# Performance work log

Hardware: AMD Instinct MI355X
Metric: run time of the kernel (lower is better)

## Reference

```python
import jax, jax.numpy as jnp
import numpy as np

IN_C, OUT_C, K, STRIDE, PAD, N_EXPERTS = 64, 128, 3, 1, 1, 4
B, H, W = 32, 64, 64


def setup_inputs() -> dict:
    key = jax.random.key(0)
    k1, k2, k3, k4 = jax.random.split(key, 4)
    x = jax.random.normal(k1, (B, IN_C, H, W), dtype=jnp.float32)
    idx = jax.random.randint(k2, (B,), 0, N_EXPERTS, dtype=jnp.int64)
    # Expert conv weights/biases (PyTorch Conv2d layout: [out_c, in_c, kh, kw])
    fan_in = IN_C * K * K
    bound = 1.0 / np.sqrt(fan_in)
    Wc = jax.random.uniform(k3, (N_EXPERTS, OUT_C, IN_C, K, K), dtype=jnp.float32,
                            minval=-bound, maxval=bound)
    bc = jax.random.uniform(k4, (N_EXPERTS, OUT_C), dtype=jnp.float32,
                            minval=-bound, maxval=bound)
    return {"x": x, "idx": idx, "Wc": Wc, "bc": bc}


def _conv2d(x, w, b):
    # x: [B, C_in, H, W], w: [C_out, C_in, K, K], b: [C_out]
    y = jax.lax.conv_general_dilated(
        x, w,
        window_strides=(STRIDE, STRIDE),
        padding=[(PAD, PAD), (PAD, PAD)],
        dimension_numbers=("NCHW", "OIHW", "NCHW"),
    )
    return y + b[None, :, None, None]


def reference(x, idx, Wc, bc):
    # Compute every expert's conv for every sample (faithful to the torch code),
    # then gather each sample's selected expert output.
    results = jax.vmap(lambda w, b: _conv2d(x, w, b))(Wc, bc)  # [E, B, C_out, H, W]
    results = jnp.moveaxis(results, 0, 1)                      # [B, E, C_out, H, W]
    out = jnp.take_along_axis(
        results, idx[:, None, None, None, None].astype(jnp.int32), axis=1
    )  # [B, 1, C_out, H, W]
    return jnp.squeeze(out, axis=1)
```

## Files before the change

kernel.cpp:

```cpp
#include <hip/hip_runtime.h>
#include <hip/hip_bf16.h>


#define IC 64
#define OC 128
#define HH 64
#define WW 64

typedef short short8 __attribute__((ext_vector_type(8)));
typedef ushort ushort8 __attribute__((ext_vector_type(8)));
typedef float float16 __attribute__((ext_vector_type(16)));

static __device__ __forceinline__ ushort f2bf(float v) {
    __hip_bfloat16 h = __float2bfloat16(v);
    return *(ushort*)&h;
}

__global__ __launch_bounds__(256)
void reorder_w(const float* __restrict__ Wc, ushort* __restrict__ wout) {
    const int u   = blockIdx.x * 256 + threadIdx.x;
    const int oc  = u & 127;
    const int ich = (u >> 7) & 7;
    const int et  = u >> 10;
    const int tap = et % 9;
    const int e   = et / 9;
    const float* src = Wc + (((size_t)(e * 128 + oc) * 64 + ich * 8) * 9 + tap);
    ushort8 v;
#pragma unroll
    for (int j = 0; j < 8; ++j) v[j] = f2bf(src[j * 9]);
    *(ushort8*)(wout + (size_t)u * 8) = v;
}

__global__ __launch_bounds__(512, 4)
void moe_conv_mfma(const float* __restrict__ x, const int* __restrict__ idx,
                   const ushort* __restrict__ wre, const float* __restrict__ bc,
                   float* __restrict__ out) {
    __shared__ __align__(16) ushort xs[6 * 8 * 66 * 8];
    __shared__ float bias[128];

    const int t    = threadIdx.x;
    const int rq   = blockIdx.x;
    const int b    = blockIdx.y;
    const int row0 = rq * 4;
    const int e    = ((unsigned)idx[b]) & 3;

    const int lane31 = t & 31;
    const int lhi    = (t >> 5) & 1;
    const int wv     = t >> 6;
    const int w0     = wv & 1;
    const int pr     = wv >> 1;

    const ushort* wsrc = wre + (size_t)e * 9 * 8192
                       + ((size_t)lhi * 128 + w0 * 64 + lane31) * 8;

    short8 a0c = *(const short8*)(wsrc);
    short8 a1c = *(const short8*)(wsrc + 256);

    if (t < 192) {
        const int r = t >> 5, rem = t & 31;
        const int ich = rem >> 2, side = (rem >> 1) & 1, q = rem & 1;
        const int hc = side ? 65 : 0;
        ushort4 z = {0, 0, 0, 0};
        *(ushort4*)&xs[(((r * 8 + ich) * 66 + hc) * 8 + q * 4)] = z;
    } else if (t < 320) {
        bias[t - 192] = bc[e * OC + (t - 192)];
    }

    const float* xb = x + (size_t)b * IC * HH * WW;
    {
        const int gc   = t & 63;
        const int csel = t >> 6;
#pragma unroll
        for (int it = 0; it < 12; ++it) {
            const int combo = it * 8 + csel;
            const int r = combo >> 4, rem = combo & 15;
            const int ich = rem >> 1, q = rem & 1;
            const int gr = row0 - 1 + r;
            ushort4 u = {0, 0, 0, 0};
            if ((unsigned)gr < (unsigned)HH) {
                const int ic0 = ich * 8 + q * 4;
                u.x = f2bf(xb[((ic0 + 0) * HH + gr) * WW + gc]);
                u.y = f2bf(xb[((ic0 + 1) * HH + gr) * WW + gc]);
                u.z = f2bf(xb[((ic0 + 2) * HH + gr) * WW + gc]);
                u.w = f2bf(xb[((ic0 + 3) * HH + gr) * WW + gc]);
            }
            *(ushort4*)&xs[(((r * 8 + ich) * 66 + (gc + 1)) * 8 + q * 4)] = u;
        }
    }

    float16 acc[2][2];
#pragma unroll
    for (int a = 0; a < 2; ++a)
#pragma unroll
        for (int cg = 0; cg < 2; ++cg)
#pragma unroll
            for (int r = 0; r < 16; ++r) acc[a][cg][r] = 0.0f;

    __syncthreads();

    const int xbase = ((pr * 8 + lhi) * 66 + lane31) * 8;

#pragma unroll
    for (int s = 0; s < 36; ++s) {
        const int tap = s >> 2, ks = s & 3;
        const int kh  = tap / 3, kw = tap - kh * 3;
        const int off = ((kh * 8 + ks * 2) * 66 + kw) * 8;

        const short8 b0 = *(const short8*)&xs[xbase + off];
        const short8 b1 = *(const short8*)&xs[xbase + off + 256];

        short8 a0n, a1n;
        if (s < 35) {
            a0n = *(const short8*)(wsrc + (s + 1) * 2048);
            a1n = *(const short8*)(wsrc + (s + 1) * 2048 + 256);
        }

        acc[0][0] = __builtin_amdgcn_mfma_f32_32x32x16_bf16(a0c, b0, acc[0][0], 0, 0, 0);
        acc[0][1] = __builtin_amdgcn_mfma_f32_32x32x16_bf16(a0c, b1, acc[0][1], 0, 0, 0);
        acc[1][0] = __builtin_amdgcn_mfma_f32_32x32x16_bf16(a1c, b0, acc[1][0], 0, 0, 0);
        acc[1][1] = __builtin_amdgcn_mfma_f32_32x32x16_bf16(a1c, b1, acc[1][1], 0, 0, 0);

        if (s < 35) { a0c = a0n; a1c = a1n; }
    }

#pragma unroll
    for (int a = 0; a < 2; ++a) {
        const int ocb = w0 * 64 + a * 32 + 4 * lhi;
#pragma unroll
        for (int reg = 0; reg < 16; ++reg) {
            const int oc = ocb + (reg & 3) + 8 * (reg >> 2);
            const float bv = bias[oc];
            const size_t base = (((size_t)b * OC + oc) * HH + (row0 + pr)) * WW;
            out[base + lane31]      = acc[a][0][reg] + bv;
            out[base + 32 + lane31] = acc[a][1][reg] + bv;
        }
    }
}

extern "C" void kernel_launch(void* const* d_in, const int* in_sizes, int n_in,
                              void* d_out, int out_size, void* d_ws, size_t ws_size,
                              hipStream_t stream) {
    const float* x   = (const float*)d_in[0];
    const int*   idx = (const int*)d_in[1];
    const float* Wc  = (const float*)d_in[2];
    const float* bc  = (const float*)d_in[3];
    float* out  = (float*)d_out;
    ushort* wre = (ushort*)d_ws;

    reorder_w<<<144, 256, 0, stream>>>(Wc, wre);
    dim3 grid(16, 32);
    moe_conv_mfma<<<grid, 512, 0, stream>>>(x, idx, wre, bc, out);
}
```

Before: 117.7 us.

## Shrink conv blocks to two rows, swizzle grid across XCDs, stage weight reorder in LDS

The conv kernel now handles two output rows per 256-thread block instead of four rows per 512 threads, giving 1024 blocks. Block IDs are remapped so consecutive blocks spread across the eight dies while keeping blocks of one sample together. The weight-reorder kernel now does coalesced loads through shared memory instead of strided gathers. MFMA issue is raised to high wave priority. Smaller blocks re-read halo rows more often, trading extra input traffic for more parallelism and better load balance.

Result: faster. 112.5 us (-4.4%).

```diff
diff --git a/kernel.cpp b/kernel.cpp
--- a/kernel.cpp
+++ b/kernel.cpp
@@ -18,30 +18,48 @@
 
 __global__ __launch_bounds__(256)
 void reorder_w(const float* __restrict__ Wc, ushort* __restrict__ wout) {
-    const int u   = blockIdx.x * 256 + threadIdx.x;
-    const int oc  = u & 127;
-    const int ich = (u >> 7) & 7;
-    const int et  = u >> 10;
-    const int tap = et % 9;
-    const int e   = et / 9;
-    const float* src = Wc + (((size_t)(e * 128 + oc) * 64 + ich * 8) * 9 + tap);
-    ushort8 v;
+    __shared__ ushort lw[4 * 584];
+    const int t   = threadIdx.x;
+    const int e   = blockIdx.x >> 5;
+    const int oc0 = (blockIdx.x & 31) * 4;
+    const float* src = Wc + (size_t)(e * 128 + oc0) * 576;
 #pragma unroll
-    for (int j = 0; j < 8; ++j) v[j] = f2bf(src[j * 9]);
-    *(ushort8*)(wout + (size_t)u * 8) = v;
+    for (int k = 0; k < 9; ++k) {
+        const int f   = k * 256 + t;
+        const int ocl = f / 576;
+        const int rem = f - ocl * 576;
+        lw[ocl * 584 + rem] = f2bf(src[f]);
+    }
+    __syncthreads();
+#pragma unroll
+    for (int k = 0; k < 2; ++k) {
+        const int n = k * 256 + t;
+        if (n < 288) {
+            const int ocl = n & 3, ich = (n >> 2) & 7, tap = n >> 5;
+            ushort8 v;
+#pragma unroll
+            for (int icl = 0; icl < 8; ++icl)
+                v[icl] = lw[ocl * 584 + (ich * 8 + icl) * 9 + tap];
+            *(ushort8*)(wout +
+                ((((size_t)(e * 9 + tap) * 8 + ich) * 128 + oc0 + ocl) * 8)) = v;
+        }
+    }
 }
 
-__global__ __launch_bounds__(512, 4)
+__global__ __launch_bounds__(256, 4)
 void moe_conv_mfma(const float* __restrict__ x, const int* __restrict__ idx,
                    const ushort* __restrict__ wre, const float* __restrict__ bc,
                    float* __restrict__ out) {
-    __shared__ __align__(16) ushort xs[6 * 8 * 66 * 8];
+    __shared__ __align__(16) ushort xs[4 * 8 * 66 * 8];
     __shared__ float bias[128];
 
-    const int t    = threadIdx.x;
-    const int rq   = blockIdx.x;
-    const int b    = blockIdx.y;
-    const int row0 = rq * 4;
+    const int t = threadIdx.x;
+
+    const int lin = blockIdx.x;
+    const int nw  = (lin & 7) * 128 + (lin >> 3);
+    const int b   = nw >> 5;
+    const int rp  = nw & 31;
+    const int row0 = rp * 2;
     const int e    = ((unsigned)idx[b]) & 3;
 
     const int lane31 = t & 31;
@@ -56,14 +74,14 @@
     short8 a0c = *(const short8*)(wsrc);
     short8 a1c = *(const short8*)(wsrc + 256);
 
-    if (t < 192) {
+    if (t < 128) {
         const int r = t >> 5, rem = t & 31;
         const int ich = rem >> 2, side = (rem >> 1) & 1, q = rem & 1;
         const int hc = side ? 65 : 0;
         ushort4 z = {0, 0, 0, 0};
         *(ushort4*)&xs[(((r * 8 + ich) * 66 + hc) * 8 + q * 4)] = z;
-    } else if (t < 320) {
-        bias[t - 192] = bc[e * OC + (t - 192)];
+    } else {
+        bias[t - 128] = bc[e * OC + (t - 128)];
     }
 
     const float* xb = x + (size_t)b * IC * HH * WW;
@@ -71,8 +89,8 @@
         const int gc   = t & 63;
         const int csel = t >> 6;
 #pragma unroll
-        for (int it = 0; it < 12; ++it) {
-            const int combo = it * 8 + csel;
+        for (int it = 0; it < 16; ++it) {
+            const int combo = it * 4 + csel;
             const int r = combo >> 4, rem = combo & 15;
             const int ich = rem >> 1, q = rem & 1;
             const int gr = row0 - 1 + r;
@@ -115,10 +133,12 @@
             a1n = *(const short8*)(wsrc + (s + 1) * 2048 + 256);
         }
 
+        __builtin_amdgcn_s_setprio(1);
         acc[0][0] = __builtin_amdgcn_mfma_f32_32x32x16_bf16(a0c, b0, acc[0][0], 0, 0, 0);
         acc[0][1] = __builtin_amdgcn_mfma_f32_32x32x16_bf16(a0c, b1, acc[0][1], 0, 0, 0);
         acc[1][0] = __builtin_amdgcn_mfma_f32_32x32x16_bf16(a1c, b0, acc[1][0], 0, 0, 0);
         acc[1][1] = __builtin_amdgcn_mfma_f32_32x32x16_bf16(a1c, b1, acc[1][1], 0, 0, 0);
+        __builtin_amdgcn_s_setprio(0);
 
         if (s < 35) { a0c = a0n; a1c = a1n; }
     }
@@ -147,7 +167,6 @@
     float* out  = (float*)d_out;
     ushort* wre = (ushort*)d_ws;
 
-    reorder_w<<<144, 256, 0, stream>>>(Wc, wre);
-    dim3 grid(16, 32);
-    moe_conv_mfma<<<grid, 512, 0, stream>>>(x, idx, wre, bc, out);
+    reorder_w<<<128, 256, 0, stream>>>(Wc, wre);
+    moe_conv_mfma<<<1024, 256, 0, stream>>>(x, idx, wre, bc, out);
 }
```
